# Kernel tuning notes

Hardware: AMD Instinct MI355X
Metric: run time of the kernel (lower is better)

Reference implementation:

```python
import jax, jax.numpy as jnp
import numpy as np
import math

B, L, Z, D, H, NL, K = 32, 64, 32, 512, 8, 8, 8192
DFF = 4 * D
HD = D // H

def _make_pe():
    pos = np.arange(L, dtype=np.float32)[:, None]
    div = np.exp(-math.log(10000.0) * np.arange(0, D, 2, dtype=np.float32) / D)
    pe = np.zeros((L, D), dtype=np.float32)
    pe[:, 0::2] = np.sin(pos * div)
    pe[:, 1::2] = np.cos(pos * div)
    return jnp.asarray(pe)

PE = _make_pe()  # (L, D) sinusoidal positional embedding, max_len = seq_len

def setup_inputs() -> dict:
    key = jax.random.key(0)
    ks = jax.random.split(key, 12)
    s = 0.02
    def rn(k, shape):
        return jax.random.normal(k, shape, jnp.float32) * s
    p = {}
    p["x"] = jax.random.normal(ks[0], (B, L, Z), jnp.float32)
    p["codebook"] = jax.random.normal(ks[1], (K, Z), jnp.float32)
    p["W_in"] = rn(ks[2], (Z, D)); p["b_in"] = jnp.zeros((D,), jnp.float32)
    p["sa_qkv_w"] = rn(ks[3], (NL, D, 3 * D)); p["sa_qkv_b"] = jnp.zeros((NL, 3 * D), jnp.float32)
    p["sa_out_w"] = rn(ks[4], (NL, D, D)); p["sa_out_b"] = jnp.zeros((NL, D), jnp.float32)
    p["ca_qkv_w"] = rn(ks[5], (NL, D, 3 * D)); p["ca_qkv_b"] = jnp.zeros((NL, 3 * D), jnp.float32)
    p["ca_out_w"] = rn(ks[6], (NL, D, D)); p["ca_out_b"] = jnp.zeros((NL, D), jnp.float32)
    p["ff1_w"] = rn(ks[7], (NL, D, DFF)); p["ff1_b"] = jnp.zeros((NL, DFF), jnp.float32)
    p["ff2_w"] = rn(ks[8], (NL, DFF, D)); p["ff2_b"] = jnp.zeros((NL, D), jnp.float32)
    p["ln1_g"] = jnp.ones((NL, D), jnp.float32); p["ln1_b"] = jnp.zeros((NL, D), jnp.float32)
    p["ln2_g"] = jnp.ones((NL, D), jnp.float32); p["ln2_b"] = jnp.zeros((NL, D), jnp.float32)
    p["ln3_g"] = jnp.ones((NL, D), jnp.float32); p["ln3_b"] = jnp.zeros((NL, D), jnp.float32)
    p["ln_g"] = jnp.ones((D,), jnp.float32); p["ln_b"] = jnp.zeros((D,), jnp.float32)
    p["W_out"] = rn(ks[9], (D, Z)); p["b_out"] = jnp.zeros((Z,), jnp.float32)
    return p

def _ln(x, g, b):
    m = x.mean(-1, keepdims=True)
    v = ((x - m) ** 2).mean(-1, keepdims=True)
    return (x - m) / jnp.sqrt(v + 1e-5) * g + b

def _mha(q_in, kv_in, qkv_w, qkv_b, out_w, out_b, key_mask):
    # q_in: (B, Lq, D), kv_in: (B, Lk, D); key_mask: (Lk,) bool or None
    q = q_in @ qkv_w[:, :D] + qkv_b[:D]
    k = kv_in @ qkv_w[:, D:2 * D] + qkv_b[D:2 * D]
    v = kv_in @ qkv_w[:, 2 * D:] + qkv_b[2 * D:]
    split = lambda t: t.reshape(t.shape[0], t.shape[1], H, HD)
    q, k, v = split(q), split(k), split(v)
    s = jnp.einsum('bqhd,bkhd->bhqk', q, k) / math.sqrt(HD)
    if key_mask is not None:
        s = jnp.where(key_mask[None, None, None, :], s, -1e9)
    a = jax.nn.softmax(s, axis=-1)
    o = jnp.einsum('bhqk,bkhd->bqhd', a, v).reshape(q_in.shape)
    return o @ out_w + out_b

def _forward(x, codebook, W_in, b_in, sa_qkv_w, sa_qkv_b, sa_out_w, sa_out_b,
             ca_qkv_w, ca_qkv_b, ca_out_w, ca_out_b, ff1_w, ff1_b, ff2_w, ff2_b,
             ln1_g, ln1_b, ln2_g, ln2_b, ln3_g, ln3_b, ln_g, ln_b, W_out, b_out):
    Bsz = x.shape[0]
    # prepend zero start token -> x_full (B, L+1, Z); context at step i = x_full[:, :i+1]
    x_full = jnp.concatenate([jnp.zeros((Bsz, 1, Z), x.dtype), x], axis=1)
    ctx_h0 = x_full[:, :L] @ W_in + b_in + PE  # padded context, fixed length L

    def step(i):
        key_mask = jnp.arange(L) <= i  # valid context positions 0..i
        # VQ nearest-neighbor quantize of the memory token x_full[:, i+1]
        mem = jnp.take(x_full, i + 1, axis=1)  # (B, Z)
        d2 = ((mem[:, None, :] - codebook[None, :, :]) ** 2).sum(-1)  # (B, K)
        q = jax.lax.stop_gradient(codebook[jnp.argmin(d2, axis=1)])  # (B, Z), detached
        mem_h = (q @ W_in + b_in)[:, None, :]  # (B, 1, D), no pos emb
        h = ctx_h0
        for l in range(NL):  # post-norm TransformerDecoderLayer, relu FFN
            sa = _mha(h, h, sa_qkv_w[l], sa_qkv_b[l], sa_out_w[l], sa_out_b[l], key_mask)
            h = _ln(h + sa, ln1_g[l], ln1_b[l])
            ca = _mha(h, mem_h, ca_qkv_w[l], ca_qkv_b[l], ca_out_w[l], ca_out_b[l], None)
            h = _ln(h + ca, ln2_g[l], ln2_b[l])
            ff = jax.nn.relu(h @ ff1_w[l] + ff1_b[l]) @ ff2_w[l] + ff2_b[l]
            h = _ln(h + ff, ln3_g[l], ln3_b[l])
        pred = _ln(h, ln_g, ln_b) @ W_out + b_out  # (B, L, Z)
        return jnp.take(pred, i, axis=1)  # last valid position (B, Z)

    preds = jax.lax.map(step, jnp.arange(L))  # (L, B, Z)
    return preds.transpose(1, 0, 2)  # (B, L, Z)

def reference(x, codebook, W_in, b_in, sa_qkv_w, sa_qkv_b, sa_out_w, sa_out_b,
              ca_qkv_w, ca_qkv_b, ca_out_w, ca_out_b, ff1_w, ff1_b, ff2_w, ff2_b,
              ln1_g, ln1_b, ln2_g, ln2_b, ln3_g, ln3_b, ln_g, ln_b, W_out, b_out):
    return _forward(x, codebook, W_in, b_in, sa_qkv_w, sa_qkv_b, sa_out_w, sa_out_b,
                    ca_qkv_w, ca_qkv_b, ca_out_w, ca_out_b, ff1_w, ff1_b, ff2_w, ff2_b,
                    ln1_g, ln1_b, ln2_g, ln2_b, ln3_g, ln3_b, ln_g, ln_b, W_out, b_out)
```

## Files before the change

kernel.cpp:

```cpp
#include <hip/hip_runtime.h>
#include <hip/hip_bf16.h>
#include <math.h>

#define DEV __device__ __forceinline__

typedef unsigned short u16;
typedef __attribute__((ext_vector_type(8))) short s8v;
typedef __attribute__((ext_vector_type(4))) float f4v;

constexpr int NLAY = 8;
constexpr int SB   = 64 * 32;
constexpr size_t RAGG = 66560;

DEV float bf2f(u16 u) { unsigned x = ((unsigned)u) << 16; union { unsigned u; float f; } c; c.u = x; return c.f; }
DEV u16 f2bf(float f) { union { float f; unsigned u; } c; c.f = f; unsigned x = c.u; x += 0x7fffu + ((x >> 16) & 1u); return (u16)(x >> 16); }

DEV void load8bf(const u16* p, float* o) {
  uint4 q = *(const uint4*)p;
  o[0] = bf2f((u16)(q.x & 0xffff)); o[1] = bf2f((u16)(q.x >> 16));
  o[2] = bf2f((u16)(q.y & 0xffff)); o[3] = bf2f((u16)(q.y >> 16));
  o[4] = bf2f((u16)(q.z & 0xffff)); o[5] = bf2f((u16)(q.z >> 16));
  o[6] = bf2f((u16)(q.w & 0xffff)); o[7] = bf2f((u16)(q.w >> 16));
}
DEV void store8bf(u16* p, const float* v) {
  uint4 q;
  q.x = (unsigned)f2bf(v[0]) | ((unsigned)f2bf(v[1]) << 16);
  q.y = (unsigned)f2bf(v[2]) | ((unsigned)f2bf(v[3]) << 16);
  q.z = (unsigned)f2bf(v[4]) | ((unsigned)f2bf(v[5]) << 16);
  q.w = (unsigned)f2bf(v[6]) | ((unsigned)f2bf(v[7]) << 16);
  *(uint4*)p = q;
}

DEV size_t seqoff(int s, int b) { return (size_t)16 * s * (s + 1) + (size_t)b * (s + 1); }

DEV void cp16(const void* g, void* l) {
  __builtin_amdgcn_global_load_lds((const __attribute__((address_space(1))) unsigned*)g,
                                   (__attribute__((address_space(3))) unsigned*)l, 16, 0, 0);
}

template<int RELU>
__global__ __launch_bounds__(256) void gemm_bt(const u16* __restrict__ A, const u16* __restrict__ Bt,
                                               const float* __restrict__ bias, u16* __restrict__ C,
                                               int N, int K) {
  __shared__ u16 As[128 * 64];
  __shared__ u16 Bs[128 * 64];
  const int tid = threadIdx.x, w = tid >> 6, lane = tid & 63;
  const int lrow = lane & 15, lquad = lane >> 4;
  const int m0 = blockIdx.y * 128, n0 = blockIdx.x * 128;
  const int wm = (w & 1) * 64, wn = (w >> 1) * 64;
  const int srow = lane >> 3, sch = (lane & 7) * 8;
  f4v acc[4][4] = {};
  for (int kt = 0; kt < K; kt += 64) {
    __syncthreads();
#pragma unroll
    for (int c = 0; c < 4; ++c) {
      int seg = w * 4 + c;
      cp16(A + (size_t)(m0 + seg * 8 + srow) * K + kt + sch, &As[seg * 512]);
      cp16(Bt + (size_t)(n0 + seg * 8 + srow) * K + kt + sch, &Bs[seg * 512]);
    }
    __syncthreads();
#pragma unroll
    for (int kc = 0; kc < 2; ++kc) {
      s8v a[4], b[4];
#pragma unroll
      for (int t = 0; t < 4; ++t) {
        a[t] = *(const s8v*)&As[(wm + t * 16 + lrow) * 64 + kc * 32 + lquad * 8];
        b[t] = *(const s8v*)&Bs[(wn + t * 16 + lrow) * 64 + kc * 32 + lquad * 8];
      }
#pragma unroll
      for (int mt = 0; mt < 4; ++mt)
#pragma unroll
        for (int nt = 0; nt < 4; ++nt)
          acc[mt][nt] = __builtin_amdgcn_mfma_f32_16x16x32_bf16(a[mt], b[nt], acc[mt][nt], 0, 0, 0);
    }
  }
#pragma unroll
  for (int nt = 0; nt < 4; ++nt) {
    int col = n0 + wn + nt * 16 + lrow;
    float bv = bias[col];
#pragma unroll
    for (int mt = 0; mt < 4; ++mt) {
      size_t rbase = (size_t)(m0 + wm + mt * 16 + lquad * 4);
#pragma unroll
      for (int j = 0; j < 4; ++j) {
        float v = acc[mt][nt][j] + bv;
        if (RELU) v = fmaxf(v, 0.f);
        C[(rbase + j) * (size_t)N + col] = f2bf(v);
      }
    }
  }
}

__global__ __launch_bounds__(256) void gemm_ca(const u16* __restrict__ A0, const u16* __restrict__ Bt0,
                                               const float* __restrict__ bias0, u16* __restrict__ C0,
                                               size_t sA, size_t sB, int sBias, size_t sC) {
  const int z = blockIdx.z;
  const u16* A = A0 + sA * z;
  const u16* Bt = Bt0 + sB * z;
  const float* bias = bias0 + (size_t)sBias * z;
  u16* C = C0 + sC * z;
  const int N = 512, K = 512;
  __shared__ u16 As[128 * 64];
  __shared__ u16 Bs[128 * 64];
  const int tid = threadIdx.x, w = tid >> 6, lane = tid & 63;
  const int lrow = lane & 15, lquad = lane >> 4;
  const int m0 = blockIdx.y * 128, n0 = blockIdx.x * 128;
  const int wm = (w & 1) * 64, wn = (w >> 1) * 64;
  const int srow = lane >> 3, sch = (lane & 7) * 8;
  f4v acc[4][4] = {};
  for (int kt = 0; kt < K; kt += 64) {
    __syncthreads();
#pragma unroll
    for (int c = 0; c < 4; ++c) {
      int seg = w * 4 + c;
      cp16(A + (size_t)(m0 + seg * 8 + srow) * K + kt + sch, &As[seg * 512]);
      cp16(Bt + (size_t)(n0 + seg * 8 + srow) * K + kt + sch, &Bs[seg * 512]);
    }
    __syncthreads();
#pragma unroll
    for (int kc = 0; kc < 2; ++kc) {
      s8v a[4], b[4];
#pragma unroll
      for (int t = 0; t < 4; ++t) {
        a[t] = *(const s8v*)&As[(wm + t * 16 + lrow) * 64 + kc * 32 + lquad * 8];
        b[t] = *(const s8v*)&Bs[(wn + t * 16 + lrow) * 64 + kc * 32 + lquad * 8];
      }
#pragma unroll
      for (int mt = 0; mt < 4; ++mt)
#pragma unroll
        for (int nt = 0; nt < 4; ++nt)
          acc[mt][nt] = __builtin_amdgcn_mfma_f32_16x16x32_bf16(a[mt], b[nt], acc[mt][nt], 0, 0, 0);
    }
  }
#pragma unroll
  for (int nt = 0; nt < 4; ++nt) {
    int col = n0 + wn + nt * 16 + lrow;
    float bv = bias[col];
#pragma unroll
    for (int mt = 0; mt < 4; ++mt) {
      size_t rbase = (size_t)(m0 + wm + mt * 16 + lquad * 4);
#pragma unroll
      for (int j = 0; j < 4; ++j)
        C[(rbase + j) * (size_t)N + col] = f2bf(acc[mt][nt][j] + bv);
    }
  }
}

__global__ __launch_bounds__(256) void k_attn(const u16* __restrict__ qkv, u16* __restrict__ o,
                                              int sbase, size_t row0) {
  const int h = blockIdx.x, b = blockIdx.y, sl = blockIdx.z;
  const int s = sbase + sl;
  const size_t soff = seqoff(s, b) - row0;
  __shared__ u16 qs[64][72], ks[64][72], vts[64][72], ps[64][72];
  const int tid = threadIdx.x;
  const int row = tid >> 2, c16 = (tid & 3) * 16;
  const int rcl = row <= s ? row : s;
  {
    const u16* qp = qkv + (soff + rcl) * 1536 + h * 64 + c16;
    *(uint4*)&qs[row][c16]     = *(const uint4*)qp;
    *(uint4*)&qs[row][c16 + 8] = *(const uint4*)(qp + 8);
    *(uint4*)&ks[row][c16]     = *(const uint4*)(qp + 512);
    *(uint4*)&ks[row][c16 + 8] = *(const uint4*)(qp + 520);
    uint4 v0 = *(const uint4*)(qp + 1024), v1 = *(const uint4*)(qp + 1032);
    unsigned arr[8] = {v0.x, v0.y, v0.z, v0.w, v1.x, v1.y, v1.z, v1.w};
#pragma unroll
    for (int j = 0; j < 8; ++j) {
      vts[c16 + 2 * j][row]     = (u16)(arr[j] & 0xffff);
      vts[c16 + 2 * j + 1][row] = (u16)(arr[j] >> 16);
    }
  }
  __syncthreads();
  const int w = tid >> 6, lane = tid & 63, lrow = lane & 15, lquad = lane >> 4;
  f4v sc[4] = {};
  {
    s8v aq[2];
#pragma unroll
    for (int kc = 0; kc < 2; ++kc) aq[kc] = *(const s8v*)&qs[w * 16 + lrow][kc * 32 + lquad * 8];
#pragma unroll
    for (int nt = 0; nt < 4; ++nt)
#pragma unroll
      for (int kc = 0; kc < 2; ++kc) {
        s8v bk = *(const s8v*)&ks[nt * 16 + lrow][kc * 32 + lquad * 8];
        sc[nt] = __builtin_amdgcn_mfma_f32_16x16x32_bf16(aq[kc], bk, sc[nt], 0, 0, 0);
      }
  }
#pragma unroll
  for (int j = 0; j < 4; ++j) {
    float v[4]; float mx = -3.0e38f;
#pragma unroll
    for (int nt = 0; nt < 4; ++nt) {
      int col = nt * 16 + lrow;
      float xx = sc[nt][j] * 0.125f;
      if (col > s) xx = -1e9f;
      v[nt] = xx; mx = fmaxf(mx, xx);
    }
#pragma unroll
    for (int m = 1; m < 16; m <<= 1) mx = fmaxf(mx, __shfl_xor(mx, m));
    float sum = 0.f;
#pragma unroll
    for (int nt = 0; nt < 4; ++nt) { v[nt] = __expf(v[nt] - mx); sum += v[nt]; }
#pragma unroll
    for (int m = 1; m < 16; m <<= 1) sum += __shfl_xor(sum, m);
    float inv = 1.f / sum;
    int prow = w * 16 + lquad * 4 + j;
#pragma unroll
    for (int nt = 0; nt < 4; ++nt) ps[prow][nt * 16 + lrow] = f2bf(v[nt] * inv);
  }
  f4v oc[4] = {};
  {
    s8v ap[2];
#pragma unroll
    for (int kc = 0; kc < 2; ++kc) ap[kc] = *(const s8v*)&ps[w * 16 + lrow][kc * 32 + lquad * 8];
#pragma unroll
    for (int nt = 0; nt < 4; ++nt)
#pragma unroll
      for (int kc = 0; kc < 2; ++kc) {
        s8v bv = *(const s8v*)&vts[nt * 16 + lrow][kc * 32 + lquad * 8];
        oc[nt] = __builtin_amdgcn_mfma_f32_16x16x32_bf16(ap[kc], bv, oc[nt], 0, 0, 0);
      }
  }
#pragma unroll
  for (int nt = 0; nt < 4; ++nt) {
    int col = h * 64 + nt * 16 + lrow;
#pragma unroll
    for (int j = 0; j < 4; ++j) {
      int r = w * 16 + lquad * 4 + j;
      if (r <= s) o[(soff + r) * 512 + col] = f2bf(oc[nt][j]);
    }
  }
}

__global__ __launch_bounds__(64) void k_attn_last(const u16* __restrict__ qb, const u16* __restrict__ kvb,
                                                  u16* __restrict__ attl, int sbase, size_t row0) {
  const int h = blockIdx.x;
  const int r = blockIdx.y;
  const int sl = r >> 5, b = r & 31;
  const int s = sbase + sl;
  const size_t soff = seqoff(s, b) - row0;
  const int lane = threadIdx.x;
  __shared__ float qsm[64], ps[64];
  qsm[lane] = bf2f(qb[(size_t)r * 512 + h * 64 + lane]);
  __syncthreads();
  float sc = -3.0e38f;
  if (lane <= s) {
    const u16* kp = kvb + (soff + lane) * 1024 + h * 64;
    float acc = 0.f;
#pragma unroll
    for (int d = 0; d < 64; d += 8) {
      float kv[8]; load8bf(kp + d, kv);
#pragma unroll
      for (int i = 0; i < 8; ++i) acc += qsm[d + i] * kv[i];
    }
    sc = acc * 0.125f;
  }
  float mx = sc;
#pragma unroll
  for (int m = 1; m < 64; m <<= 1) mx = fmaxf(mx, __shfl_xor(mx, m));
  float e = (lane <= s) ? __expf(sc - mx) : 0.f;
  float sum = e;
#pragma unroll
  for (int m = 1; m < 64; m <<= 1) sum += __shfl_xor(sum, m);
  ps[lane] = e / sum;
  __syncthreads();
  float acc = 0.f;
  for (int k = 0; k <= s; ++k)
    acc += ps[k] * bf2f(kvb[(soff + k) * 1024 + 512 + h * 64 + lane]);
  attl[(size_t)r * 512 + h * 64 + lane] = f2bf(acc);
}

template<int HAS2>
__global__ __launch_bounds__(256) void k_ln(u16* __restrict__ hb, const u16* __restrict__ tmpb,
                                            const u16* __restrict__ cab, const int* __restrict__ map,
                                            size_t row0,
                                            const float* __restrict__ g1, const float* __restrict__ b1,
                                            const float* __restrict__ g2, const float* __restrict__ b2) {
  const int row = blockIdx.x * 4 + (threadIdx.x >> 6);
  const int lane = threadIdx.x & 63;
  const size_t off = (size_t)row * 512 + lane * 8;
  float hv[8], tv[8], t[8];
  load8bf(hb + off, hv); load8bf(tmpb + off, tv);
  float s = 0.f, ss = 0.f;
#pragma unroll
  for (int i = 0; i < 8; ++i) { t[i] = hv[i] + tv[i]; s += t[i]; ss += t[i] * t[i]; }
#pragma unroll
  for (int m = 1; m < 64; m <<= 1) { s += __shfl_xor(s, m); ss += __shfl_xor(ss, m); }
  float mean = s * (1.f / 512.f);
  float inv = 1.f / sqrtf(ss * (1.f / 512.f) - mean * mean + 1e-5f);
  float gv[8], bv[8];
  *(float4*)&gv[0] = *(const float4*)(g1 + lane * 8); *(float4*)&gv[4] = *(const float4*)(g1 + lane * 8 + 4);
  *(float4*)&bv[0] = *(const float4*)(b1 + lane * 8); *(float4*)&bv[4] = *(const float4*)(b1 + lane * 8 + 4);
  if (HAS2) {
    const int seq = map[row0 + row];
    float cv[8]; load8bf(cab + (size_t)seq * 512 + lane * 8, cv);
    float s2 = 0.f, ss2 = 0.f;
#pragma unroll
    for (int i = 0; i < 8; ++i) { float n = (t[i] - mean) * inv * gv[i] + bv[i] + cv[i]; t[i] = n; s2 += n; ss2 += n * n; }
#pragma unroll
    for (int m = 1; m < 64; m <<= 1) { s2 += __shfl_xor(s2, m); ss2 += __shfl_xor(ss2, m); }
    float mean2 = s2 * (1.f / 512.f);
    float inv2 = 1.f / sqrtf(ss2 * (1.f / 512.f) - mean2 * mean2 + 1e-5f);
    float g2v[8], b2v[8];
    *(float4*)&g2v[0] = *(const float4*)(g2 + lane * 8); *(float4*)&g2v[4] = *(const float4*)(g2 + lane * 8 + 4);
    *(float4*)&b2v[0] = *(const float4*)(b2 + lane * 8); *(float4*)&b2v[4] = *(const float4*)(b2 + lane * 8 + 4);
#pragma unroll
    for (int i = 0; i < 8; ++i) t[i] = (t[i] - mean2) * inv2 * g2v[i] + b2v[i];
  } else {
#pragma unroll
    for (int i = 0; i < 8; ++i) t[i] = (t[i] - mean) * inv * gv[i] + bv[i];
  }
  store8bf(hb + off, t);
}

template<int HAS2>
__global__ __launch_bounds__(256) void k_ln_last(u16* __restrict__ gl, const u16* __restrict__ tmpl,
                                                 const u16* __restrict__ cab, int sbase,
                                                 const float* __restrict__ g1, const float* __restrict__ b1,
                                                 const float* __restrict__ g2, const float* __restrict__ b2) {
  const int row = blockIdx.x * 4 + (threadIdx.x >> 6);
  const int lane = threadIdx.x & 63;
  const size_t off = (size_t)row * 512 + lane * 8;
  float hv[8], tv[8], t[8];
  load8bf(gl + off, hv); load8bf(tmpl + off, tv);
  float s = 0.f, ss = 0.f;
#pragma unroll
  for (int i = 0; i < 8; ++i) { t[i] = hv[i] + tv[i]; s += t[i]; ss += t[i] * t[i]; }
#pragma unroll
  for (int m = 1; m < 64; m <<= 1) { s += __shfl_xor(s, m); ss += __shfl_xor(ss, m); }
  float mean = s * (1.f / 512.f);
  float inv = 1.f / sqrtf(ss * (1.f / 512.f) - mean * mean + 1e-5f);
  float gv[8], bv[8];
  *(float4*)&gv[0] = *(const float4*)(g1 + lane * 8); *(float4*)&gv[4] = *(const float4*)(g1 + lane * 8 + 4);
  *(float4*)&bv[0] = *(const float4*)(b1 + lane * 8); *(float4*)&bv[4] = *(const float4*)(b1 + lane * 8 + 4);
  if (HAS2) {
    const int seq = (sbase + (row >> 5)) * 32 + (row & 31);
    float cv[8]; load8bf(cab + (size_t)seq * 512 + lane * 8, cv);
    float s2 = 0.f, ss2 = 0.f;
#pragma unroll
    for (int i = 0; i < 8; ++i) { float n = (t[i] - mean) * inv * gv[i] + bv[i] + cv[i]; t[i] = n; s2 += n; ss2 += n * n; }
#pragma unroll
    for (int m = 1; m < 64; m <<= 1) { s2 += __shfl_xor(s2, m); ss2 += __shfl_xor(ss2, m); }
    float mean2 = s2 * (1.f / 512.f);
    float inv2 = 1.f / sqrtf(ss2 * (1.f / 512.f) - mean2 * mean2 + 1e-5f);
    float g2v[8], b2v[8];
    *(float4*)&g2v[0] = *(const float4*)(g2 + lane * 8); *(float4*)&g2v[4] = *(const float4*)(g2 + lane * 8 + 4);
    *(float4*)&b2v[0] = *(const float4*)(b2 + lane * 8); *(float4*)&b2v[4] = *(const float4*)(b2 + lane * 8 + 4);
#pragma unroll
    for (int i = 0; i < 8; ++i) t[i] = (t[i] - mean2) * inv2 * g2v[i] + b2v[i];
  } else {
#pragma unroll
    for (int i = 0; i < 8; ++i) t[i] = (t[i] - mean) * inv * gv[i] + bv[i];
  }
  store8bf(gl + off, t);
}

__global__ __launch_bounds__(256) void k_ctx(const float* __restrict__ x, const float* __restrict__ W_in,
                                             const float* __restrict__ b_in, u16* __restrict__ ctx0) {
  const int e = blockIdx.x * 256 + threadIdx.x;
  const int d = e & 511, l = (e >> 9) & 63, b = e >> 15;
  float acc = b_in[d];
  if (l > 0) {
    const float* xr = x + (size_t)(b * 64 + l - 1) * 32;
#pragma unroll 8
    for (int z = 0; z < 32; ++z) acc += xr[z] * W_in[z * 512 + d];
  }
  const float dv = __expf(-9.210340371976184f * (float)(d & ~1) * (1.f / 512.f));
  const float ang = (float)l * dv;
  acc += (d & 1) ? cosf(ang) : sinf(ang);
  ctx0[(size_t)e] = f2bf(acc);
}

__global__ __launch_bounds__(64) void k_map(int* __restrict__ map) {
  const int seq = blockIdx.x;
  const int s = seq >> 5, b = seq & 31;
  const int l = threadIdx.x;
  if (l <= s) map[seqoff(s, b) + l] = seq;
}

__global__ __launch_bounds__(256) void k_rep(const u16* __restrict__ ctx0, u16* __restrict__ hb,
                                             int sbase, size_t row0) {
  const int sl = blockIdx.x >> 5, b = blockIdx.x & 31;
  const int s = sbase + sl;
  const size_t dst0 = seqoff(s, b) - row0;
  const int tid = threadIdx.x;
  for (int idx = tid; idx < (s + 1) * 64; idx += 256) {
    const int l = idx >> 6, d8 = idx & 63;
    *(uint4*)(hb + (dst0 + l) * 512 + d8 * 8) =
        *(const uint4*)(ctx0 + ((size_t)(b * 64 + l) * 512) + d8 * 8);
  }
}

__global__ __launch_bounds__(64) void k_gather(const u16* __restrict__ hb, u16* __restrict__ gl,
                                               int sbase, size_t row0) {
  const int r = blockIdx.x; const int sl = r >> 5, b = r & 31; const int s = sbase + sl;
  const size_t src = (seqoff(s, b) - row0 + s) * 512;
  const int lane = threadIdx.x;
  *(uint4*)(gl + (size_t)r * 512 + lane * 8) = *(const uint4*)(hb + src + lane * 8);
}

__global__ __launch_bounds__(256) void k_vq(const float* __restrict__ x, const float* __restrict__ cb,
                                            const float* __restrict__ W_in, const float* __restrict__ b_in,
                                            u16* __restrict__ memh) {
  const int tok = blockIdx.x;
  const int s = tok >> 5, b = tok & 31;
  const int tid = threadIdx.x;
  __shared__ float xs[32], cs[32];
  __shared__ float rd[256]; __shared__ int ri[256];
  if (tid < 32) xs[tid] = x[(size_t)(b * 64 + s) * 32 + tid];
  __syncthreads();
  float xr[32];
#pragma unroll
  for (int i = 0; i < 32; ++i) xr[i] = xs[i];
  float bd = 3.0e38f; int bi = 0;
#pragma unroll 2
  for (int c = tid; c < 8192; c += 256) {
    const float4* cr = (const float4*)(cb + (size_t)c * 32);
    float d0 = 0.f, d1 = 0.f, d2 = 0.f, d3 = 0.f;
#pragma unroll
    for (int z4 = 0; z4 < 8; ++z4) {
      float4 cv = cr[z4];
      float t0 = xr[z4 * 4 + 0] - cv.x, t1 = xr[z4 * 4 + 1] - cv.y;
      float t2 = xr[z4 * 4 + 2] - cv.z, t3 = xr[z4 * 4 + 3] - cv.w;
      d0 += t0 * t0; d1 += t1 * t1; d2 += t2 * t2; d3 += t3 * t3;
    }
    float d = (d0 + d1) + (d2 + d3);
    if (d < bd) { bd = d; bi = c; }
  }
  rd[tid] = bd; ri[tid] = bi;
  __syncthreads();
  for (int st = 128; st > 0; st >>= 1) {
    if (tid < st) {
      float dn = rd[tid + st]; int in2 = ri[tid + st];
      if (dn < rd[tid] || (dn == rd[tid] && in2 < ri[tid])) { rd[tid] = dn; ri[tid] = in2; }
    }
    __syncthreads();
  }
  const int kmin = ri[0];
  if (tid < 32) cs[tid] = cb[(size_t)kmin * 32 + tid];
  __syncthreads();
  for (int o = tid; o < 512; o += 256) {
    float a = b_in[o];
#pragma unroll 8
    for (int z = 0; z < 32; ++z) a += cs[z] * W_in[z * 512 + o];
    memh[(size_t)tok * 512 + o] = f2bf(a);
  }
}

__global__ __launch_bounds__(64) void k_final(const u16* __restrict__ gl, const float* __restrict__ g,
                                              const float* __restrict__ bta, const float* __restrict__ Wout,
                                              const float* __restrict__ bout, float* __restrict__ out,
                                              int sbase) {
  const int blk = blockIdx.x;
  const int s = sbase + (blk >> 5), b = blk & 31;
  const int lane = threadIdx.x;
  __shared__ float ns[512];
  const size_t roff = (size_t)blk * 512;
  float v[8]; load8bf(gl + roff + lane * 8, v);
  float sm = 0.f, ssm = 0.f;
#pragma unroll
  for (int i = 0; i < 8; ++i) { sm += v[i]; ssm += v[i] * v[i]; }
#pragma unroll
  for (int m = 1; m < 64; m <<= 1) { sm += __shfl_xor(sm, m); ssm += __shfl_xor(ssm, m); }
  float mean = sm * (1.f / 512.f);
  float inv = 1.f / sqrtf(ssm * (1.f / 512.f) - mean * mean + 1e-5f);
#pragma unroll
  for (int i = 0; i < 8; ++i) ns[lane * 8 + i] = (v[i] - mean) * inv * g[lane * 8 + i] + bta[lane * 8 + i];
  __syncthreads();
  const int col = lane & 31, half = lane >> 5;
  float a = 0.f;
  for (int k = half * 256; k < half * 256 + 256; ++k) a += ns[k] * Wout[(size_t)k * 32 + col];
  a += __shfl_xor(a, 32);
  if (lane < 32) out[((size_t)b * 64 + s) * 32 + col] = a + bout[col];
}

__global__ void k_tcast(const float* __restrict__ src, u16* __restrict__ dst, int R, int C, int ld, int col0) {
  const int l = blockIdx.z;
  src += (size_t)l * R * ld;
  dst += (size_t)l * R * C;
  __shared__ float t[32][33];
  const int c0 = blockIdx.x * 32, r0 = blockIdx.y * 32;
  const int tx = threadIdx.x, ty = threadIdx.y;
#pragma unroll
  for (int k = 0; k < 4; ++k)
    t[ty + 8 * k][tx] = src[(size_t)(r0 + ty + 8 * k) * ld + col0 + c0 + tx];
  __syncthreads();
#pragma unroll
  for (int k = 0; k < 4; ++k)
    dst[(size_t)(c0 + ty + 8 * k) * R + r0 + tx] = f2bf(t[tx][ty + 8 * k]);
}

extern "C" void kernel_launch(void* const* d_in, const int* in_sizes, int n_in,
                              void* d_out, int out_size, void* d_ws, size_t ws_size,
                              hipStream_t stream) {
  (void)in_sizes; (void)n_in; (void)out_size;
  const float* x    = (const float*)d_in[0];
  const float* cb   = (const float*)d_in[1];
  const float* W_in = (const float*)d_in[2];
  const float* b_in = (const float*)d_in[3];
  const float* saqw = (const float*)d_in[4];
  const float* saqb = (const float*)d_in[5];
  const float* saow = (const float*)d_in[6];
  const float* saob = (const float*)d_in[7];
  const float* caqw = (const float*)d_in[8];
  const float* caqb = (const float*)d_in[9];
  const float* caow = (const float*)d_in[10];
  const float* caob = (const float*)d_in[11];
  const float* f1w  = (const float*)d_in[12];
  const float* f1b  = (const float*)d_in[13];
  const float* f2w  = (const float*)d_in[14];
  const float* f2b  = (const float*)d_in[15];
  const float* l1g  = (const float*)d_in[16];
  const float* l1b  = (const float*)d_in[17];
  const float* l2g  = (const float*)d_in[18];
  const float* l2b  = (const float*)d_in[19];
  const float* l3g  = (const float*)d_in[20];
  const float* l3b  = (const float*)d_in[21];
  const float* lng  = (const float*)d_in[22];
  const float* lnb  = (const float*)d_in[23];
  const float* Wout = (const float*)d_in[24];
  const float* bout = (const float*)d_in[25];
  float* out = (float*)d_out;

  u16* ws = (u16*)d_ws;
  size_t off = 0;
  auto alloc = [&](size_t n) { u16* p = ws + off; off += n; return p; };
  u16* ctx0  = alloc((size_t)32 * 64 * 512);
  u16* cabuf = alloc((size_t)NLAY * SB * 512);
  u16* memh  = alloc((size_t)SB * 512);
  u16* tmpv8 = alloc((size_t)NLAY * SB * 512);
  u16* wqkvT = alloc((size_t)NLAY * 1536 * 512);
  u16* woutT = alloc((size_t)NLAY * 512 * 512);
  u16* wf1T  = alloc((size_t)NLAY * 2048 * 512);
  u16* wf2T  = alloc((size_t)NLAY * 512 * 2048);
  u16* wcavT = alloc((size_t)NLAY * 512 * 512);
  u16* wcaoT = alloc((size_t)NLAY * 512 * 512);
  int* rowmap = (int*)alloc(RAGG * 2);

  u16* glast = tmpv8;
  u16* qb    = tmpv8 + 1048576;
  u16* attl  = tmpv8 + 2 * 1048576;
  u16* tmpl  = tmpv8 + 3 * 1048576;
  u16* midl  = tmpv8 + 4 * 1048576;

  size_t avail = ws_size / 2 > off ? ws_size / 2 - off : 0;
  size_t Ralloc = avail / 3072;
  Ralloc = Ralloc / 128 * 128;
  if (Ralloc > RAGG) Ralloc = RAGG;

  u16* hb   = alloc(Ralloc * 512);
  u16* regA = alloc(Ralloc * 2048);
  u16* tmpb = alloc(Ralloc * 512);
  u16* qkvb = regA;
  u16* attb = regA + Ralloc * 1536;
  u16* midb = regA;
  u16* kvb  = regA;

  dim3 tb(32, 8);
  k_tcast<<<dim3(48, 16, 8), tb, 0, stream>>>(saqw, wqkvT, 512, 1536, 1536, 0);
  k_tcast<<<dim3(16, 16, 8), tb, 0, stream>>>(saow, woutT, 512, 512, 512, 0);
  k_tcast<<<dim3(64, 16, 8), tb, 0, stream>>>(f1w, wf1T, 512, 2048, 2048, 0);
  k_tcast<<<dim3(16, 64, 8), tb, 0, stream>>>(f2w, wf2T, 2048, 512, 512, 0);
  k_tcast<<<dim3(16, 16, 8), tb, 0, stream>>>(caqw, wcavT, 512, 512, 1536, 1024);
  k_tcast<<<dim3(16, 16, 8), tb, 0, stream>>>(caow, wcaoT, 512, 512, 512, 0);

  k_ctx<<<4096, 256, 0, stream>>>(x, W_in, b_in, ctx0);
  k_vq<<<2048, 256, 0, stream>>>(x, cb, W_in, b_in, memh);
  k_map<<<2048, 64, 0, stream>>>(rowmap);

  gemm_ca<<<dim3(4, 16, 8), 256, 0, stream>>>(memh, wcavT, caqb + 1024, tmpv8,
                                              0, (size_t)512 * 512, 1536, (size_t)SB * 512);
  gemm_ca<<<dim3(4, 16, 8), 256, 0, stream>>>(tmpv8, wcaoT, caob, cabuf,
                                              (size_t)SB * 512, (size_t)512 * 512, 512, (size_t)SB * 512);

  int sstart = 0;
  while (sstart < 64) {
    int send = sstart;
    size_t rows = 0;
    while (send < 64) {
      size_t nr = rows + (size_t)32 * (send + 1);
      size_t pr = (nr + 127) / 128 * 128;
      if (pr > Ralloc && send > sstart) break;
      rows = nr; ++send;
      if (pr > Ralloc) break;
    }
    const size_t row0 = (size_t)16 * sstart * (sstart + 1);
    const size_t rows_pad = (rows + 127) / 128 * 128;
    const int mg = (int)(rows_pad / 128);
    const int ns = send - sstart;
    const int nseq = ns * 32;
    const int nseqp = (nseq + 127) / 128 * 128;

    k_rep<<<nseq, 256, 0, stream>>>(ctx0, hb, sstart, row0);
    for (int l = 0; l < NLAY - 1; ++l) {
      gemm_bt<0><<<dim3(12, mg), 256, 0, stream>>>(hb, wqkvT + (size_t)l * 1536 * 512,
                                                   saqb + (size_t)l * 1536, qkvb, 1536, 512);
      k_attn<<<dim3(8, 32, ns), 256, 0, stream>>>(qkvb, attb, sstart, row0);
      gemm_bt<0><<<dim3(4, mg), 256, 0, stream>>>(attb, woutT + (size_t)l * 512 * 512,
                                                  saob + (size_t)l * 512, tmpb, 512, 512);
      k_ln<1><<<(int)(rows / 4), 256, 0, stream>>>(hb, tmpb, cabuf + (size_t)l * SB * 512,
                                                   rowmap, row0,
                                                   l1g + l * 512, l1b + l * 512, l2g + l * 512, l2b + l * 512);
      gemm_bt<1><<<dim3(16, mg), 256, 0, stream>>>(hb, wf1T + (size_t)l * 2048 * 512,
                                                   f1b + (size_t)l * 2048, midb, 2048, 512);
      gemm_bt<0><<<dim3(4, mg), 256, 0, stream>>>(midb, wf2T + (size_t)l * 512 * 2048,
                                                  f2b + (size_t)l * 512, tmpb, 512, 2048);
      k_ln<0><<<(int)(rows / 4), 256, 0, stream>>>(hb, tmpb, nullptr, rowmap, row0,
                                                   l3g + l * 512, l3b + l * 512, nullptr, nullptr);
    }
    {
      const size_t l7q = (size_t)7 * 1536 * 512;
      k_gather<<<nseq, 64, 0, stream>>>(hb, glast, sstart, row0);
      gemm_bt<0><<<dim3(8, mg), 256, 0, stream>>>(hb, wqkvT + l7q + (size_t)512 * 512,
                                                  saqb + 7 * 1536 + 512, kvb, 1024, 512);
      gemm_bt<0><<<dim3(4, nseqp / 128), 256, 0, stream>>>(glast, wqkvT + l7q,
                                                           saqb + 7 * 1536, qb, 512, 512);
      k_attn_last<<<dim3(8, nseq), 64, 0, stream>>>(qb, kvb, attl, sstart, row0);
      gemm_bt<0><<<dim3(4, nseqp / 128), 256, 0, stream>>>(attl, woutT + (size_t)7 * 512 * 512,
                                                           saob + 7 * 512, tmpl, 512, 512);
      k_ln_last<1><<<nseq / 4, 256, 0, stream>>>(glast, tmpl, cabuf + (size_t)7 * SB * 512, sstart,
                                                 l1g + 7 * 512, l1b + 7 * 512, l2g + 7 * 512, l2b + 7 * 512);
      gemm_bt<1><<<dim3(16, nseqp / 128), 256, 0, stream>>>(glast, wf1T + (size_t)7 * 2048 * 512,
                                                            f1b + (size_t)7 * 2048, midl, 2048, 512);
      gemm_bt<0><<<dim3(4, nseqp / 128), 256, 0, stream>>>(midl, wf2T + (size_t)7 * 512 * 2048,
                                                           f2b + 7 * 512, tmpl, 512, 2048);
      k_ln_last<0><<<nseq / 4, 256, 0, stream>>>(glast, tmpl, nullptr, sstart,
                                                 l3g + 7 * 512, l3b + 7 * 512, nullptr, nullptr);
      k_final<<<nseq, 64, 0, stream>>>(glast, lng, lnb, Wout, bout, out, sstart);
    }
    sstart = send;
  }
}
```

Baseline: 7.550 ms.

## Tile codebook through shared memory and process eight tokens per VQ block

The VQ nearest-codebook kernel now handles 8 tokens per block, staging 128-entry codebook tiles in shared memory so each tile is reused across tokens. The argmin is packed as a 64-bit (distance, index) key and reduced with wave shuffles instead of a shared-memory tree. The input projection in k_ctx also splits its dot product into four independent accumulators. These cut redundant global codebook reads and barrier-heavy reductions, but the grid drops from 2048 to 256 blocks, and the kernel is a small part of the total time.

```diff
diff --git a/kernel.cpp b/kernel.cpp
--- a/kernel.cpp
+++ b/kernel.cpp
@@ -1,6 +1,7 @@
 #include <hip/hip_runtime.h>
 #include <hip/hip_bf16.h>
 #include <math.h>
+#include <string.h>
 
 #define DEV __device__ __forceinline__
 
@@ -360,8 +361,15 @@
   float acc = b_in[d];
   if (l > 0) {
     const float* xr = x + (size_t)(b * 64 + l - 1) * 32;
-#pragma unroll 8
-    for (int z = 0; z < 32; ++z) acc += xr[z] * W_in[z * 512 + d];
+    float a0 = 0.f, a1 = 0.f, a2 = 0.f, a3 = 0.f;
+#pragma unroll
+    for (int z = 0; z < 32; z += 4) {
+      a0 += xr[z + 0] * W_in[(z + 0) * 512 + d];
+      a1 += xr[z + 1] * W_in[(z + 1) * 512 + d];
+      a2 += xr[z + 2] * W_in[(z + 2) * 512 + d];
+      a3 += xr[z + 3] * W_in[(z + 3) * 512 + d];
+    }
+    acc += (a0 + a1) + (a2 + a3);
   }
   const float dv = __expf(-9.210340371976184f * (float)(d & ~1) * (1.f / 512.f));
   const float ang = (float)l * dv;
@@ -400,47 +408,60 @@
 __global__ __launch_bounds__(256) void k_vq(const float* __restrict__ x, const float* __restrict__ cb,
                                             const float* __restrict__ W_in, const float* __restrict__ b_in,
                                             u16* __restrict__ memh) {
-  const int tok = blockIdx.x;
+  __shared__ float cs[128 * 36];
+  __shared__ float xs[8][33];
+  const int tid = threadIdx.x;
+  const int g = tid >> 5, u = tid & 31;
+  const int tok = blockIdx.x * 8 + g;
   const int s = tok >> 5, b = tok & 31;
-  const int tid = threadIdx.x;
-  __shared__ float xs[32], cs[32];
-  __shared__ float rd[256]; __shared__ int ri[256];
-  if (tid < 32) xs[tid] = x[(size_t)(b * 64 + s) * 32 + tid];
+  xs[g][u] = x[(size_t)(b * 64 + s) * 32 + u];
   __syncthreads();
   float xr[32];
 #pragma unroll
-  for (int i = 0; i < 32; ++i) xr[i] = xs[i];
-  float bd = 3.0e38f; int bi = 0;
-#pragma unroll 2
-  for (int c = tid; c < 8192; c += 256) {
-    const float4* cr = (const float4*)(cb + (size_t)c * 32);
-    float d0 = 0.f, d1 = 0.f, d2 = 0.f, d3 = 0.f;
-#pragma unroll
-    for (int z4 = 0; z4 < 8; ++z4) {
-      float4 cv = cr[z4];
-      float t0 = xr[z4 * 4 + 0] - cv.x, t1 = xr[z4 * 4 + 1] - cv.y;
-      float t2 = xr[z4 * 4 + 2] - cv.z, t3 = xr[z4 * 4 + 3] - cv.w;
-      d0 += t0 * t0; d1 += t1 * t1; d2 += t2 * t2; d3 += t3 * t3;
-    }
-    float d = (d0 + d1) + (d2 + d3);
-    if (d < bd) { bd = d; bi = c; }
-  }
-  rd[tid] = bd; ri[tid] = bi;
-  __syncthreads();
-  for (int st = 128; st > 0; st >>= 1) {
-    if (tid < st) {
-      float dn = rd[tid + st]; int in2 = ri[tid + st];
-      if (dn < rd[tid] || (dn == rd[tid] && in2 < ri[tid])) { rd[tid] = dn; ri[tid] = in2; }
-    }
+  for (int i = 0; i < 32; ++i) xr[i] = xs[g][i];
+  unsigned long long bk = ~0ull;
+  for (int tile = 0; tile < 64; ++tile) {
     __syncthreads();
-  }
-  const int kmin = ri[0];
-  if (tid < 32) cs[tid] = cb[(size_t)kmin * 32 + tid];
-  __syncthreads();
-  for (int o = tid; o < 512; o += 256) {
+    const float4* src = (const float4*)(cb + (size_t)tile * 128 * 32);
+#pragma unroll
+    for (int k = 0; k < 4; ++k) {
+      int f4 = k * 256 + tid;
+      int c = f4 >> 3, z = (f4 & 7) * 4;
+      *(float4*)&cs[c * 36 + z] = src[f4];
+    }
+    __syncthreads();
+#pragma unroll
+    for (int j = 0; j < 4; ++j) {
+      int c = j * 32 + u;
+      const float* cp = &cs[c * 36];
+      float d0 = 0.f, d1 = 0.f, d2 = 0.f, d3 = 0.f;
+#pragma unroll
+      for (int z4 = 0; z4 < 8; ++z4) {
+        float4 cv = *(const float4*)(cp + z4 * 4);
+        float t0 = xr[z4 * 4 + 0] - cv.x, t1 = xr[z4 * 4 + 1] - cv.y;
+        float t2 = xr[z4 * 4 + 2] - cv.z, t3 = xr[z4 * 4 + 3] - cv.w;
+        d0 += t0 * t0; d1 += t1 * t1; d2 += t2 * t2; d3 += t3 * t3;
+      }
+      float d = (d0 + d1) + (d2 + d3);
+      unsigned db; memcpy(&db, &d, 4);
+      unsigned long long key = ((unsigned long long)db << 32) | (unsigned)(tile * 128 + c);
+      bk = key < bk ? key : bk;
+    }
+  }
+#pragma unroll
+  for (int m = 1; m < 32; m <<= 1) {
+    unsigned long long o = __shfl_xor(bk, m);
+    bk = o < bk ? o : bk;
+  }
+  const int kmin = (int)(bk & 0xffffffffu);
+  float cw[32];
+#pragma unroll
+  for (int z = 0; z < 32; ++z) cw[z] = cb[(size_t)kmin * 32 + z];
+  for (int k = 0; k < 16; ++k) {
+    int o = u + 32 * k;
     float a = b_in[o];
-#pragma unroll 8
-    for (int z = 0; z < 32; ++z) a += cs[z] * W_in[z * 512 + o];
+#pragma unroll
+    for (int z = 0; z < 32; ++z) a += cw[z] * W_in[z * 512 + o];
     memh[(size_t)tok * 512 + o] = f2bf(a);
   }
 }
@@ -563,7 +584,7 @@
   k_tcast<<<dim3(16, 16, 8), tb, 0, stream>>>(caow, wcaoT, 512, 512, 512, 0);
 
   k_ctx<<<4096, 256, 0, stream>>>(x, W_in, b_in, ctx0);
-  k_vq<<<2048, 256, 0, stream>>>(x, cb, W_in, b_in, memh);
+  k_vq<<<256, 256, 0, stream>>>(x, cb, W_in, b_in, memh);
   k_map<<<2048, 64, 0, stream>>>(rowmap);
 
   gemm_ca<<<dim3(4, 16, 8), 256, 0, stream>>>(memh, wcavT, caqb + 1024, tmpv8,
```

Result: no change. 7.414 ms (-1.8%).
